# Kernel tuning notes

Measured on AMD Instinct MI355X. Metric: run time of the kernel, lower is better.

The kernel has to match this reference:

```python
import jax, jax.numpy as jnp
import numpy as np

N = 100000       # nodes
E = 3200000      # edges (avg degree 32)
IN_F = 256
OUT_F = 128
LRELU_ALPHA = 0.2
EPS = 1e-16


def setup_inputs() -> dict:
    key = jax.random.key(0)
    k1, k2, k3, k4 = jax.random.split(key, 4)
    x = jax.random.normal(k1, (N, IN_F), dtype=jnp.float32)
    edge_index = jax.random.randint(k2, (2, E), 0, N, dtype=jnp.int32)
    # xavier_uniform with gain=calculate_gain('relu')=sqrt(2)
    gain = float(np.sqrt(2.0))
    bw = gain * float(np.sqrt(6.0 / (IN_F + OUT_F)))
    weight = jax.random.uniform(k3, (IN_F, OUT_F), dtype=jnp.float32, minval=-bw, maxval=bw)
    ba = gain * float(np.sqrt(6.0 / (1 + 2 * OUT_F)))
    a = jax.random.uniform(k4, (1, 2 * OUT_F), dtype=jnp.float32, minval=-ba, maxval=ba)
    return {"x": x, "edge_index": edge_index, "weight": weight, "a": a}


def reference(x, edge_index, weight, a):
    src = edge_index[0]
    dst = edge_index[1]
    h = x @ weight                                  # [N, OUT_F]
    # e_edge = a @ cat(h[src], h[dst]) == (h @ a_l)[src] + (h @ a_r)[dst]
    a_l = a[0, :OUT_F]
    a_r = a[0, OUT_F:]
    s_l = h @ a_l                                   # [N]
    s_r = h @ a_r                                   # [N]
    e = s_l[src] + s_r[dst]                         # [E]
    e = jnp.where(e >= 0, e, LRELU_ALPHA * e)       # LeakyReLU
    # segment softmax over src groups
    e_max = jax.ops.segment_max(e, src, num_segments=N)   # [N]
    e_exp = jnp.exp(e - e_max[src])                        # [E]
    denom = jax.ops.segment_sum(e_exp, src, num_segments=N)[src] + EPS
    alpha_e = e_exp / denom                                # [E]
    # out[src] += alpha_e * h[dst]  (sparse A_alpha @ h)
    out = jax.ops.segment_sum(alpha_e[:, None] * h[dst], src, num_segments=N)
    return out
```

## Files before the change

kernel.cpp:

```cpp
#include <hip/hip_runtime.h>

#define GN 100000
#define GE 3200000
#define CAP 128
#define NB 391
#define CHUNK 4096

typedef __attribute__((ext_vector_type(8))) short bf16x8;
typedef __attribute__((ext_vector_type(4))) float f32x4;

__device__ __forceinline__ unsigned short f2bf(float f) {
    unsigned u = __float_as_uint(f);
    u += 0x7fffu + ((u >> 16) & 1u);
    return (unsigned short)(u >> 16);
}
__device__ __forceinline__ float bf2f(unsigned short u) {
    return __uint_as_float(((unsigned)u) << 16);
}

__global__ __launch_bounds__(256) void wprep_kernel(const float* __restrict__ w,
                                                    unsigned short* __restrict__ wT) {
    int flat4 = blockIdx.x * 256 + threadIdx.x;
    if (flat4 >= 256 * 128 / 4) return;
    int k  = flat4 >> 5;
    int n4 = (flat4 & 31) * 4;
    float4 v = ((const float4*)w)[flat4];
    wT[(size_t)(n4 + 0) * 256 + k] = f2bf(v.x);
    wT[(size_t)(n4 + 1) * 256 + k] = f2bf(v.y);
    wT[(size_t)(n4 + 2) * 256 + k] = f2bf(v.z);
    wT[(size_t)(n4 + 3) * 256 + k] = f2bf(v.w);
}

__global__ __launch_bounds__(256) void gemm_kernel(const float* __restrict__ x,
                                                   const unsigned short* __restrict__ wT,
                                                   const float* __restrict__ a,
                                                   unsigned short* __restrict__ hq,
                                                   float* __restrict__ s_l,
                                                   float* __restrict__ s_r) {
    __shared__ unsigned short As[128][40];
    const int tid  = threadIdx.x;
    const int lane = tid & 63, wid = tid >> 6;
    const int l16  = lane & 15, quad = lane >> 4;
    const int wm   = (wid >> 1) * 64, wn = (wid & 1) * 64;
    const int bm   = blockIdx.x * 128;

    f32x4 acc[4][4] = {};

    const int arow = tid >> 1, ahalf = tid & 1;
    int gr = bm + arow; if (gr >= GN) gr = GN - 1;
    const float* xrow = x + (size_t)gr * 256 + ahalf * 16;

    for (int k0 = 0; k0 < 256; k0 += 32) {
        float4 f0 = *(const float4*)(xrow + k0);
        float4 f1 = *(const float4*)(xrow + k0 + 4);
        float4 f2 = *(const float4*)(xrow + k0 + 8);
        float4 f3 = *(const float4*)(xrow + k0 + 12);
        bf16x8 s0, s1;
        s0[0] = f2bf(f0.x); s0[1] = f2bf(f0.y); s0[2] = f2bf(f0.z); s0[3] = f2bf(f0.w);
        s0[4] = f2bf(f1.x); s0[5] = f2bf(f1.y); s0[6] = f2bf(f1.z); s0[7] = f2bf(f1.w);
        s1[0] = f2bf(f2.x); s1[1] = f2bf(f2.y); s1[2] = f2bf(f2.z); s1[3] = f2bf(f2.w);
        s1[4] = f2bf(f3.x); s1[5] = f2bf(f3.y); s1[6] = f2bf(f3.z); s1[7] = f2bf(f3.w);
        __syncthreads();
        *(bf16x8*)&As[arow][ahalf * 16]     = s0;
        *(bf16x8*)&As[arow][ahalf * 16 + 8] = s1;
        __syncthreads();
        bf16x8 af[4], bfr[4];
#pragma unroll
        for (int t = 0; t < 4; ++t) {
            af[t]  = *(const bf16x8*)&As[wm + t * 16 + l16][quad * 8];
            bfr[t] = *(const bf16x8*)(wT + (size_t)(wn + t * 16 + l16) * 256 + k0 + quad * 8);
        }
#pragma unroll
        for (int ti = 0; ti < 4; ++ti)
#pragma unroll
            for (int tj = 0; tj < 4; ++tj)
                acc[ti][tj] = __builtin_amdgcn_mfma_f32_16x16x32_bf16(af[ti], bfr[tj], acc[ti][tj], 0, 0, 0);
    }

    float alv[4], arv[4];
#pragma unroll
    for (int tj = 0; tj < 4; ++tj) {
        alv[tj] = a[wn + tj * 16 + l16];
        arv[tj] = a[128 + wn + tj * 16 + l16];
    }
#pragma unroll
    for (int ti = 0; ti < 4; ++ti) {
        float slp[4], srp[4];
#pragma unroll
        for (int r = 0; r < 4; ++r) {
            int row = bm + wm + ti * 16 + quad * 4 + r;
            float v0 = acc[ti][0][r], v1 = acc[ti][1][r], v2 = acc[ti][2][r], v3 = acc[ti][3][r];
            if (row < GN) {
                unsigned short* hp = hq + (size_t)row * 128 + wn + l16;
                hp[0]  = f2bf(v0);
                hp[16] = f2bf(v1);
                hp[32] = f2bf(v2);
                hp[48] = f2bf(v3);
            }
            slp[r] = v0 * alv[0] + v1 * alv[1] + v2 * alv[2] + v3 * alv[3];
            srp[r] = v0 * arv[0] + v1 * arv[1] + v2 * arv[2] + v3 * arv[3];
        }
#pragma unroll
        for (int off = 1; off < 16; off <<= 1)
#pragma unroll
            for (int r = 0; r < 4; ++r) {
                slp[r] += __shfl_xor(slp[r], off, 64);
                srp[r] += __shfl_xor(srp[r], off, 64);
            }
        if (l16 == 0) {
#pragma unroll
            for (int r = 0; r < 4; ++r) {
                int row = bm + wm + ti * 16 + quad * 4 + r;
                if (row < GN) {
                    atomicAdd(&s_l[row], slp[r]);
                    atomicAdd(&s_r[row], srp[r]);
                }
            }
        }
    }
}

__global__ __launch_bounds__(256) void bhist_kernel(const int* __restrict__ src,
                                                    int* __restrict__ bcnt) {
    __shared__ int bh[NB];
    const int tid = threadIdx.x;
    for (int j = tid; j < NB; j += 256) bh[j] = 0;
    __syncthreads();
    const int base = blockIdx.x * CHUNK;
    const int cnt = min(CHUNK, GE - base);
    for (int i = tid; i < cnt; i += 256) atomicAdd(&bh[src[base + i] >> 8], 1);
    __syncthreads();
    for (int j = tid; j < NB; j += 256)
        if (bh[j]) atomicAdd(&bcnt[j], bh[j]);
}

__global__ __launch_bounds__(64) void bscan_kernel(const int* __restrict__ bcnt,
                                                   int* __restrict__ bbase,
                                                   int* __restrict__ bcursor) {
    __shared__ int arr[NB];
    const int tid = threadIdx.x;
    for (int j = tid; j < NB; j += 64) arr[j] = bcnt[j];
    __syncthreads();
    int carry = 0;
    for (int b0 = 0; b0 < NB; b0 += 64) {
        int idx = b0 + tid;
        int v = (idx < NB) ? arr[idx] : 0;
        int x = v;
#pragma unroll
        for (int off = 1; off < 64; off <<= 1) {
            int y = __shfl_up(x, off, 64);
            if (tid >= off) x += y;
        }
        if (idx < NB) { bbase[idx] = carry + x - v; bcursor[idx] = carry + x - v; }
        carry += __shfl(x, 63, 64);
    }
    if (tid == 0) bbase[NB] = carry;
}

__global__ __launch_bounds__(256) void bin_kernel(const int* __restrict__ ei,
                                                  int* __restrict__ bcursor,
                                                  unsigned* __restrict__ binned) {
    __shared__ int h_cnt[NB];
    __shared__ int h_base[NB + 1];
    __shared__ int h_gpos[NB];
    __shared__ int h_cur[NB];
    __shared__ unsigned sbuf[CHUNK];
    const int tid = threadIdx.x;
    const int base = blockIdx.x * CHUNK;
    const int cnt = min(CHUNK, GE - base);

    int srcv[CHUNK / 256], dstv[CHUNK / 256];
#pragma unroll
    for (int i = 0; i < CHUNK / 256; ++i) {
        int idx = tid + i * 256;
        if (idx < cnt) { srcv[i] = ei[base + idx]; dstv[i] = ei[GE + base + idx]; }
        else srcv[i] = -1;
    }
    for (int j = tid; j < NB; j += 256) h_cnt[j] = 0;
    __syncthreads();
#pragma unroll
    for (int i = 0; i < CHUNK / 256; ++i)
        if (srcv[i] >= 0) atomicAdd(&h_cnt[srcv[i] >> 8], 1);
    __syncthreads();
    if (tid < 64) {
        int carry = 0;
        for (int b0 = 0; b0 < NB; b0 += 64) {
            int idx = b0 + tid;
            int v = (idx < NB) ? h_cnt[idx] : 0;
            int x = v;
#pragma unroll
            for (int off = 1; off < 64; off <<= 1) {
                int y = __shfl_up(x, off, 64);
                if (tid >= off) x += y;
            }
            if (idx < NB) h_base[idx] = carry + x - v;
            carry += __shfl(x, 63, 64);
        }
        if (tid == 0) h_base[NB] = carry;
    }
    __syncthreads();
    for (int j = tid; j < NB; j += 256) {
        h_cur[j] = h_base[j];
        int c = h_cnt[j];
        if (c) h_gpos[j] = atomicAdd(&bcursor[j], c);
    }
    __syncthreads();
#pragma unroll
    for (int i = 0; i < CHUNK / 256; ++i)
        if (srcv[i] >= 0) {
            int b = srcv[i] >> 8;
            int p = atomicAdd(&h_cur[b], 1);
            sbuf[p] = ((unsigned)(srcv[i] & 255) << 17) | (unsigned)dstv[i];
        }
    __syncthreads();
    for (int p = tid; p < cnt; p += 256) {
        int lo = 0, hi = NB - 1;
        while (lo < hi) {
            int mid = (lo + hi + 1) >> 1;
            if (h_base[mid] <= p) lo = mid; else hi = mid - 1;
        }
        binned[h_gpos[lo] + (p - h_base[lo])] = sbuf[p];
    }
}

__global__ __launch_bounds__(256) void fine_kernel(const unsigned* __restrict__ binned,
                                                   const int* __restrict__ bbase,
                                                   int* __restrict__ rowptr,
                                                   int* __restrict__ adj) {
    __shared__ int n_cnt[256];
    __shared__ int n_base[257];
    __shared__ int n_cur[256];
    const int b = blockIdx.x;
    const int tid = threadIdx.x;
    const int node0 = b * 256;
    const int nn = min(256, GN - node0);
    const int beg = bbase[b], end = bbase[b + 1];
    n_cnt[tid] = 0;
    __syncthreads();
    for (int p = beg + tid; p < end; p += 256)
        atomicAdd(&n_cnt[binned[p] >> 17], 1);
    __syncthreads();
    if (tid < 64) {
        int carry = 0;
        for (int b0 = 0; b0 < 256; b0 += 64) {
            int idx = b0 + tid;
            int v = n_cnt[idx];
            int x = v;
#pragma unroll
            for (int off = 1; off < 64; off <<= 1) {
                int y = __shfl_up(x, off, 64);
                if (tid >= off) x += y;
            }
            n_base[idx] = carry + x - v;
            carry += __shfl(x, 63, 64);
        }
        if (tid == 0) n_base[256] = carry;
    }
    __syncthreads();
    if (tid < nn) rowptr[node0 + tid] = beg + n_base[tid];
    if (b == NB - 1 && tid == 0) rowptr[GN] = end;
    n_cur[tid] = n_base[tid];
    __syncthreads();
    for (int p = beg + tid; p < end; p += 256) {
        unsigned e = binned[p];
        int s = e >> 17, d = (int)(e & 0x1FFFFu);
        int pos = atomicAdd(&n_cur[s], 1);
        adj[beg + pos] = d;
    }
}

__global__ __launch_bounds__(256) void aggregate_kernel(const ushort2* __restrict__ h2,
                                                        const float* __restrict__ s_l,
                                                        const float* __restrict__ s_r,
                                                        const int* __restrict__ rowptr,
                                                        const int* __restrict__ adj,
                                                        float* __restrict__ out) {
    __shared__ int   s_dst[4][CAP];
    __shared__ float s_al[4][CAP];
    const int wid = threadIdx.x >> 6, lane = threadIdx.x & 63;
    const int node = blockIdx.x * 4 + wid;
    const int beg = rowptr[node], end = rowptr[node + 1];
    const int deg = end - beg;
    const float sl = s_l[node];

    float m = -1e30f, d = 0.f;
    for (int j = lane; j < deg; j += 64) {
        int dst = adj[beg + j];
        float e = sl + s_r[dst];
        e = (e >= 0.f) ? e : 0.2f * e;
        if (j < CAP) { s_dst[wid][j] = dst; s_al[wid][j] = e; }
        float mn = fmaxf(m, e);
        d = d * __expf(m - mn) + __expf(e - mn);
        m = mn;
    }
#pragma unroll
    for (int off = 32; off; off >>= 1) {
        float m2 = __shfl_xor(m, off, 64);
        float d2 = __shfl_xor(d, off, 64);
        float mn = fmaxf(m, m2);
        d = d * __expf(m - mn) + d2 * __expf(m2 - mn);
        m = mn;
    }
    float inv = 1.f / (d + 1e-16f);
    __syncthreads();
    const int n2 = deg < CAP ? deg : CAP;
    for (int j = lane; j < n2; j += 64)
        s_al[wid][j] = __expf(s_al[wid][j] - m) * inv;
    __syncthreads();

    float2 acc = {0.f, 0.f};
    int j = 0;
    for (; j + 4 <= n2; j += 4) {
        int   d0 = s_dst[wid][j],      d1 = s_dst[wid][j + 1];
        int   d2i = s_dst[wid][j + 2], d3 = s_dst[wid][j + 3];
        float a0 = s_al[wid][j],       a1 = s_al[wid][j + 1];
        float a2 = s_al[wid][j + 2],   a3 = s_al[wid][j + 3];
        ushort2 v0 = h2[(size_t)d0 * 64 + lane];
        ushort2 v1 = h2[(size_t)d1 * 64 + lane];
        ushort2 v2 = h2[(size_t)d2i * 64 + lane];
        ushort2 v3 = h2[(size_t)d3 * 64 + lane];
        acc.x += a0 * bf2f(v0.x) + a1 * bf2f(v1.x) + a2 * bf2f(v2.x) + a3 * bf2f(v3.x);
        acc.y += a0 * bf2f(v0.y) + a1 * bf2f(v1.y) + a2 * bf2f(v2.y) + a3 * bf2f(v3.y);
    }
    for (; j < n2; ++j) {
        int d0 = s_dst[wid][j]; float a0 = s_al[wid][j];
        ushort2 v0 = h2[(size_t)d0 * 64 + lane];
        acc.x += a0 * bf2f(v0.x); acc.y += a0 * bf2f(v0.y);
    }
    for (; j < deg; ++j) {
        int dst = adj[beg + j];
        float e = sl + s_r[dst];
        e = (e >= 0.f) ? e : 0.2f * e;
        float a0 = __expf(e - m) * inv;
        ushort2 v0 = h2[(size_t)dst * 64 + lane];
        acc.x += a0 * bf2f(v0.x); acc.y += a0 * bf2f(v0.y);
    }
    ((float2*)out)[(size_t)node * 64 + lane] = acc;
}

extern "C" void kernel_launch(void* const* d_in, const int* in_sizes, int n_in,
                              void* d_out, int out_size, void* d_ws, size_t ws_size,
                              hipStream_t stream) {
    const float* x  = (const float*)d_in[0];
    const int*   ei = (const int*)d_in[1];
    const float* w  = (const float*)d_in[2];
    const float* a  = (const float*)d_in[3];
    float* out = (float*)d_out;

    unsigned short* hq = (unsigned short*)d_ws;
    float* s_l     = (float*)(hq + (size_t)GN * 128);
    float* s_r     = s_l + GN;
    int*   bcnt    = (int*)(s_r + GN);
    int*   bbase   = bcnt + NB;
    int*   bcursor = bbase + NB + 1;
    int*   rowptr  = bcursor + NB;
    unsigned* binned = (unsigned*)(rowptr + GN + 1);
    int*   adj     = (int*)(binned + GE);
    unsigned short* wT = (unsigned short*)(adj + GE);

    hipMemsetAsync(s_l, 0, (size_t)(2 * GN + NB) * sizeof(float), stream);

    wprep_kernel<<<32, 256, 0, stream>>>(w, wT);
    gemm_kernel<<<(GN + 127) / 128, 256, 0, stream>>>(x, wT, a, hq, s_l, s_r);
    bhist_kernel<<<(GE + CHUNK - 1) / CHUNK, 256, 0, stream>>>(ei, bcnt);
    bscan_kernel<<<1, 64, 0, stream>>>(bcnt, bbase, bcursor);
    bin_kernel<<<(GE + CHUNK - 1) / CHUNK, 256, 0, stream>>>(ei, bcursor, binned);
    fine_kernel<<<NB, 256, 0, stream>>>(binned, bbase, rowptr, adj);
    aggregate_kernel<<<GN / 4, 256, 0, stream>>>((const ushort2*)hq, s_l, s_r, rowptr, adj, out);
}
```

Before: 413.0 us.

## Gather bf16 rows with 16-byte loads over four edges per wave, two-pass softmax

The aggregate kernel now splits each wave into four 16-lane groups. Each group gathers a full bf16 row of h with uint4 loads, so the wave handles four edges per iteration instead of one edge per wave with 4-byte loads. A cross-group shuffle reduction merges the partial sums, and normalisation is applied once at the end. The online softmax is replaced by a max pass followed by an exp-sum pass, with dst and weight packed into int2 in shared memory. The bin kernel records each edge's global position during scatter, which removes the per-element binary search at the cost of extra shared memory.

Result: no change. 410.4 us (-0.6%).

```diff
diff --git a/kernel.cpp b/kernel.cpp
--- a/kernel.cpp
+++ b/kernel.cpp
@@ -13,9 +13,6 @@
     unsigned u = __float_as_uint(f);
     u += 0x7fffu + ((u >> 16) & 1u);
     return (unsigned short)(u >> 16);
-}
-__device__ __forceinline__ float bf2f(unsigned short u) {
-    return __uint_as_float(((unsigned)u) << 16);
 }
 
 __global__ __launch_bounds__(256) void wprep_kernel(const float* __restrict__ w,
@@ -165,6 +162,7 @@
     __shared__ int h_gpos[NB];
     __shared__ int h_cur[NB];
     __shared__ unsigned sbuf[CHUNK];
+    __shared__ int sgpos[CHUNK];
     const int tid = threadIdx.x;
     const int base = blockIdx.x * CHUNK;
     const int cnt = min(CHUNK, GE - base);
@@ -211,16 +209,11 @@
             int b = srcv[i] >> 8;
             int p = atomicAdd(&h_cur[b], 1);
             sbuf[p] = ((unsigned)(srcv[i] & 255) << 17) | (unsigned)dstv[i];
-        }
-    __syncthreads();
-    for (int p = tid; p < cnt; p += 256) {
-        int lo = 0, hi = NB - 1;
-        while (lo < hi) {
-            int mid = (lo + hi + 1) >> 1;
-            if (h_base[mid] <= p) lo = mid; else hi = mid - 1;
-        }
-        binned[h_gpos[lo] + (p - h_base[lo])] = sbuf[p];
-    }
+            sgpos[p] = h_gpos[b] + (p - h_base[b]);
+        }
+    __syncthreads();
+    for (int p = tid; p < cnt; p += 256)
+        binned[sgpos[p]] = sbuf[p];
 }
 
 __global__ __launch_bounds__(256) void fine_kernel(const unsigned* __restrict__ binned,
@@ -269,73 +262,106 @@
     }
 }
 
-__global__ __launch_bounds__(256) void aggregate_kernel(const ushort2* __restrict__ h2,
+__global__ __launch_bounds__(256) void aggregate_kernel(const uint4* __restrict__ h4,
                                                         const float* __restrict__ s_l,
                                                         const float* __restrict__ s_r,
                                                         const int* __restrict__ rowptr,
                                                         const int* __restrict__ adj,
                                                         float* __restrict__ out) {
-    __shared__ int   s_dst[4][CAP];
-    __shared__ float s_al[4][CAP];
+    __shared__ int2 s_da[4][CAP];
     const int wid = threadIdx.x >> 6, lane = threadIdx.x & 63;
     const int node = blockIdx.x * 4 + wid;
     const int beg = rowptr[node], end = rowptr[node + 1];
     const int deg = end - beg;
     const float sl = s_l[node];
 
-    float m = -1e30f, d = 0.f;
+    float m = -1e30f;
     for (int j = lane; j < deg; j += 64) {
         int dst = adj[beg + j];
         float e = sl + s_r[dst];
         e = (e >= 0.f) ? e : 0.2f * e;
-        if (j < CAP) { s_dst[wid][j] = dst; s_al[wid][j] = e; }
-        float mn = fmaxf(m, e);
-        d = d * __expf(m - mn) + __expf(e - mn);
-        m = mn;
-    }
-#pragma unroll
-    for (int off = 32; off; off >>= 1) {
-        float m2 = __shfl_xor(m, off, 64);
-        float d2 = __shfl_xor(d, off, 64);
-        float mn = fmaxf(m, m2);
-        d = d * __expf(m - mn) + d2 * __expf(m2 - mn);
-        m = mn;
-    }
-    float inv = 1.f / (d + 1e-16f);
-    __syncthreads();
+        if (j < CAP) { int2 t; t.x = dst; t.y = __float_as_int(e); s_da[wid][j] = t; }
+        m = fmaxf(m, e);
+    }
+#pragma unroll
+    for (int off = 1; off < 64; off <<= 1)
+        m = fmaxf(m, __shfl_xor(m, off, 64));
+    __syncthreads();
+
     const int n2 = deg < CAP ? deg : CAP;
-    for (int j = lane; j < n2; j += 64)
-        s_al[wid][j] = __expf(s_al[wid][j] - m) * inv;
-    __syncthreads();
-
-    float2 acc = {0.f, 0.f};
-    int j = 0;
-    for (; j + 4 <= n2; j += 4) {
-        int   d0 = s_dst[wid][j],      d1 = s_dst[wid][j + 1];
-        int   d2i = s_dst[wid][j + 2], d3 = s_dst[wid][j + 3];
-        float a0 = s_al[wid][j],       a1 = s_al[wid][j + 1];
-        float a2 = s_al[wid][j + 2],   a3 = s_al[wid][j + 3];
-        ushort2 v0 = h2[(size_t)d0 * 64 + lane];
-        ushort2 v1 = h2[(size_t)d1 * 64 + lane];
-        ushort2 v2 = h2[(size_t)d2i * 64 + lane];
-        ushort2 v3 = h2[(size_t)d3 * 64 + lane];
-        acc.x += a0 * bf2f(v0.x) + a1 * bf2f(v1.x) + a2 * bf2f(v2.x) + a3 * bf2f(v3.x);
-        acc.y += a0 * bf2f(v0.y) + a1 * bf2f(v1.y) + a2 * bf2f(v2.y) + a3 * bf2f(v3.y);
-    }
-    for (; j < n2; ++j) {
-        int d0 = s_dst[wid][j]; float a0 = s_al[wid][j];
-        ushort2 v0 = h2[(size_t)d0 * 64 + lane];
-        acc.x += a0 * bf2f(v0.x); acc.y += a0 * bf2f(v0.y);
-    }
-    for (; j < deg; ++j) {
+    float d = 0.f;
+    for (int j = lane; j < n2; j += 64) {
+        float w = __expf(__int_as_float(s_da[wid][j].y) - m);
+        s_da[wid][j].y = __float_as_int(w);
+        d += w;
+    }
+    for (int j = CAP + lane; j < deg; j += 64) {
         int dst = adj[beg + j];
         float e = sl + s_r[dst];
         e = (e >= 0.f) ? e : 0.2f * e;
-        float a0 = __expf(e - m) * inv;
-        ushort2 v0 = h2[(size_t)dst * 64 + lane];
-        acc.x += a0 * bf2f(v0.x); acc.y += a0 * bf2f(v0.y);
-    }
-    ((float2*)out)[(size_t)node * 64 + lane] = acc;
+        d += __expf(e - m);
+    }
+#pragma unroll
+    for (int off = 1; off < 64; off <<= 1)
+        d += __shfl_xor(d, off, 64);
+    const float inv = 1.f / (d + 1e-16f);
+    __syncthreads();
+
+    const int fl = lane & 15, grp = lane >> 4;
+    f32x4 accA = {0.f, 0.f, 0.f, 0.f}, accB = {0.f, 0.f, 0.f, 0.f};
+    int j = 0;
+#pragma unroll 2
+    for (; j < n2; j += 4) {
+        int jj = j + grp;
+        bool act = jj < n2;
+        int2 da = s_da[wid][act ? jj : 0];
+        float w = act ? __int_as_float(da.y) : 0.f;
+        uint4 v = h4[(size_t)da.x * 16 + fl];
+        accA.x += w * __uint_as_float(v.x << 16);
+        accA.y += w * __uint_as_float(v.x & 0xffff0000u);
+        accA.z += w * __uint_as_float(v.y << 16);
+        accA.w += w * __uint_as_float(v.y & 0xffff0000u);
+        accB.x += w * __uint_as_float(v.z << 16);
+        accB.y += w * __uint_as_float(v.z & 0xffff0000u);
+        accB.z += w * __uint_as_float(v.w << 16);
+        accB.w += w * __uint_as_float(v.w & 0xffff0000u);
+    }
+    for (; j < deg; j += 4) {
+        int jj = j + grp;
+        bool act = jj < deg;
+        int dst = act ? adj[beg + jj] : 0;
+        float e = sl + s_r[dst];
+        e = (e >= 0.f) ? e : 0.2f * e;
+        float w = act ? __expf(e - m) : 0.f;
+        uint4 v = h4[(size_t)dst * 16 + fl];
+        accA.x += w * __uint_as_float(v.x << 16);
+        accA.y += w * __uint_as_float(v.x & 0xffff0000u);
+        accA.z += w * __uint_as_float(v.y << 16);
+        accA.w += w * __uint_as_float(v.y & 0xffff0000u);
+        accB.x += w * __uint_as_float(v.z << 16);
+        accB.y += w * __uint_as_float(v.z & 0xffff0000u);
+        accB.z += w * __uint_as_float(v.w << 16);
+        accB.w += w * __uint_as_float(v.w & 0xffff0000u);
+    }
+
+#pragma unroll
+    for (int off = 16; off < 64; off <<= 1) {
+        accA.x += __shfl_xor(accA.x, off, 64);
+        accA.y += __shfl_xor(accA.y, off, 64);
+        accA.z += __shfl_xor(accA.z, off, 64);
+        accA.w += __shfl_xor(accA.w, off, 64);
+        accB.x += __shfl_xor(accB.x, off, 64);
+        accB.y += __shfl_xor(accB.y, off, 64);
+        accB.z += __shfl_xor(accB.z, off, 64);
+        accB.w += __shfl_xor(accB.w, off, 64);
+    }
+    if (lane < 16) {
+        float* orow = out + (size_t)node * 128 + fl * 8;
+        accA.x *= inv; accA.y *= inv; accA.z *= inv; accA.w *= inv;
+        accB.x *= inv; accB.y *= inv; accB.z *= inv; accB.w *= inv;
+        *(f32x4*)orow       = accA;
+        *(f32x4*)(orow + 4) = accB;
+    }
 }
 
 extern "C" void kernel_launch(void* const* d_in, const int* in_sizes, int n_in,
@@ -366,5 +392,5 @@
     bscan_kernel<<<1, 64, 0, stream>>>(bcnt, bbase, bcursor);
     bin_kernel<<<(GE + CHUNK - 1) / CHUNK, 256, 0, stream>>>(ei, bcursor, binned);
     fine_kernel<<<NB, 256, 0, stream>>>(binned, bbase, rowptr, adj);
-    aggregate_kernel<<<GN / 4, 256, 0, stream>>>((const ushort2*)hq, s_l, s_r, rowptr, adj, out);
-}
+    aggregate_kernel<<<GN / 4, 256, 0, stream>>>((const uint4*)hq, s_l, s_r, rowptr, adj, out);
+}
```
